# Kernel optimization log

Hardware: AMD Instinct MI355X
Metric: run time of the kernel (lower is better)

## Reference

```python
import jax, jax.numpy as jnp
import numpy as np
import math

N = 5000; K = 30; E = N * K
C_S, C_Z, C_A = 256, 128, 16
H, DH, P, L = 4, 64, 8, 4
NUM_AA = 21
NUM_RBF = 16; D_MIN, D_MAX = 2.0, 22.0
EPS = 1e-8

def _ln(x):
    mu = jnp.mean(x, -1, keepdims=True)
    var = jnp.mean((x - mu) ** 2, -1, keepdims=True)
    return (x - mu) * jax.lax.rsqrt(var + 1e-5)

def _inv_apply(rot, trans, x):
    # rigid invert_apply: R^T (x - t); rot [n,3,3], trans [n,3], x [n,p,3]
    return jnp.einsum('nji,npj->npi', rot, x - trans[:, None, :])

def _rbf(d):
    mu = jnp.linspace(D_MIN, D_MAX, NUM_RBF)
    sigma = (D_MAX - D_MIN) / NUM_RBF
    return jnp.exp(-(((d[..., None] - mu) / sigma) ** 2))

def _dihedral_feats(bb):
    X = bb.reshape(-1, 3)  # [3N,3] N,CA,C chain
    dX = X[1:] - X[:-1]
    U = dX / (jnp.linalg.norm(dX, axis=-1, keepdims=True) + EPS)
    u2, u1, u0 = U[:-2], U[1:-1], U[2:]
    n2 = jnp.cross(u2, u1); n2 = n2 / (jnp.linalg.norm(n2, axis=-1, keepdims=True) + EPS)
    n1 = jnp.cross(u1, u0); n1 = n1 / (jnp.linalg.norm(n1, axis=-1, keepdims=True) + EPS)
    cosD = jnp.clip(jnp.sum(n2 * n1, -1), -1 + 1e-7, 1 - 1e-7)
    D = jnp.sign(jnp.sum(u2 * n1, -1)) * jnp.arccos(cosD)
    D = jnp.pad(D, (1, 2)).reshape(-1, 3)  # [N,3]
    return jnp.concatenate([jnp.cos(D), jnp.sin(D)], -1)  # [N,6]

def _virtual_cb(n, ca, c):
    b = ca - n; cc = c - ca; a = jnp.cross(b, cc)
    return -0.58273431 * a + 0.56802827 * b - 0.54067466 * cc + ca

def _prep(seq, atom14, rot, trans, res_mask, mgm_mask, noising_mask, atom14_exists, edge_index, atom_tab):
    res_f = res_mask.astype(jnp.float32)
    mgm_f = mgm_mask.astype(jnp.float32)
    bb = atom14[:, :3]
    dih = _dihedral_feats(bb)
    seq_oh = jax.nn.one_hot(seq, NUM_AA)
    node_vec = _inv_apply(rot, trans, atom14[:, :4])  # [N,4,3]
    node_raw = jnp.concatenate([dih, mgm_f[:, None], seq_oh * mgm_f[:, None], node_vec.reshape(N, -1)], -1) * res_f[:, None]
    sc = jnp.where(jnp.arange(14) >= 4, mgm_f[:, None], 1.0)  # zero hidden side-chain atoms
    am_f = jnp.where(jnp.arange(14) >= 4, mgm_mask[:, None], atom14_exists).astype(jnp.float32)
    atom_raw = atom_tab[seq] * sc[..., None]  # [N,14,9]
    dsti, srci = edge_index[0], edge_index[1]
    nsrc = noising_mask[srci].astype(jnp.float32); ndst = noising_mask[dsti].astype(jnp.float32)
    cb = _virtual_cb(bb[:, 0], bb[:, 1], bb[:, 2])
    bb4 = jnp.concatenate([bb, cb[:, None]], 1)  # [N,4,3]
    dist = jnp.linalg.norm(bb4[srci][:, :, None] - bb4[dsti][:, None, :] + EPS, axis=-1)  # [E,4,4]
    rbf = _rbf(dist).reshape(E, -1)  # [E,256]
    dpos = (dsti - srci).astype(jnp.float32)
    freq = jnp.exp(jnp.arange(0, 16, 2, dtype=jnp.float32) * (-math.log(10000.0) / 16))
    ang = dpos[:, None] * freq
    pe = jnp.concatenate([jnp.cos(ang), jnp.sin(ang)], -1)  # [E,16]
    bb_local = _inv_apply(rot, trans, bb4)
    src_local = bb_local[srci].reshape(E, -1) * (1 - nsrc)[:, None]
    dst_in_src = jnp.einsum('eji,epj->epi', rot[srci], bb4[dsti] - trans[srci][:, None, :]).reshape(E, -1) * (1 - ndst)[:, None]
    edge_mask = res_mask[srci] & res_mask[dsti]
    edge_raw = jnp.concatenate([ndst[:, None], nsrc[:, None], seq_oh[srci] * (1 - nsrc)[:, None], seq_oh[dsti] * (1 - ndst)[:, None], rbf, pe, src_local, dst_in_src], -1) * edge_mask.astype(jnp.float32)[:, None]
    return node_raw, edge_raw, atom_raw, res_f, am_f, edge_mask

def _mlp3(x, W1, W2, W3):
    return _ln(jax.nn.relu(jax.nn.relu(x @ W1) @ W2) @ W3)

def _net(node_raw, edge_raw, atom_raw, res_f, am_f, edge_mask, rot, trans, edge_index, Wn1, Wn2, Wn3, Wez1, Wez2, Wez3, Wa1, Wa2, Wa3, Wq, Wk, Wv, Wqp, Wkp, Wb, gamma, Wo, Wau, Wt1, Wt2, Wne, We1, We2, Wp1, Wp2, Wmu, Wlv):
    s = _mlp3(node_raw, Wn1, Wn2, Wn3)    # [N,256]
    z = _mlp3(edge_raw, Wez1, Wez2, Wez3) # [E,128]
    af = _mlp3(atom_raw, Wa1, Wa2, Wa3)   # [N,14,16]
    dsti, srci = edge_index[0], edge_index[1]
    em_f = edge_mask.astype(jnp.float32)
    w_pt = math.sqrt(2.0 / (9 * P)); w_l = math.sqrt(1.0 / 3.0)
    for l in range(L):
        q = (s @ Wq[l]).reshape(N, H, DH); k = (s @ Wk[l]).reshape(N, H, DH); v = (s @ Wv[l]).reshape(N, H, DH)
        qp = (s @ Wqp[l]).reshape(N, H, P, 3); kp = (s @ Wkp[l]).reshape(N, H, P, 3)
        qg = jnp.einsum('nij,nhpj->nhpi', rot, qp) + trans[:, None, None, :]
        kg = jnp.einsum('nij,nhpj->nhpi', rot, kp) + trans[:, None, None, :]
        logits = (jnp.sum(q[dsti] * k[srci], -1) * (w_l / math.sqrt(DH))
                  + w_l * (z @ Wb[l])
                  - 0.5 * w_pt * jax.nn.softplus(gamma[l]) * jnp.sum((qg[dsti] - kg[srci]) ** 2, (-2, -1)))
        logits = jnp.where(edge_mask[:, None], logits, -1e9)
        m = jax.ops.segment_max(logits, dsti, num_segments=N)
        a = jnp.exp(logits - m[dsti]) * em_f[:, None]
        a = a / (jax.ops.segment_sum(a, dsti, num_segments=N) + 1e-9)[dsti]
        ov = jax.ops.segment_sum(a[..., None] * v[srci], dsti, num_segments=N).reshape(N, -1)
        og = jax.ops.segment_sum(a[..., None, None] * kg[srci], dsti, num_segments=N)
        ol = jnp.einsum('nji,nhpj->nhpi', rot, og - trans[:, None, None, :])
        on = jnp.sqrt(jnp.sum(ol ** 2, -1) + EPS)
        s = _ln(s + jnp.concatenate([ov, ol.reshape(N, -1), on.reshape(N, -1)], -1) @ Wo[l])
        af = _ln(af + jnp.concatenate([af, jnp.broadcast_to(s[:, None, :], (N, 14, C_S))], -1) @ Wau[l])
        s = _ln(s + jax.nn.relu(s @ Wt1[l]) @ Wt2[l]) * res_f[:, None]
        h = s @ Wne[l]
        z = _ln(jax.nn.relu(jnp.concatenate([z, h[dsti], h[srci]], -1) @ We1[l]) @ We2[l]) * em_f[:, None]
        af = _ln(af + jax.nn.relu(af @ Wp1[l]) @ Wp2[l]) * am_f[..., None]
    return jnp.concatenate([s @ Wmu, s @ Wlv], -1)  # [N,512] = [mu | logvar]

def setup_inputs():
    ks = jax.random.split(jax.random.key(0), 40)
    w = lambda i, shp: jax.random.normal(ks[i], shp, dtype=jnp.float32) * 0.02
    return {
        'seq': jax.random.randint(ks[0], (N,), 0, NUM_AA, dtype=jnp.int32),
        'atom14': jax.random.normal(ks[1], (N, 14, 3), dtype=jnp.float32) * 3.0,
        'rot': jax.random.normal(ks[2], (N, 3, 3), dtype=jnp.float32),
        'trans': jax.random.normal(ks[3], (N, 3), dtype=jnp.float32) * 3.0,
        'res_mask': jnp.ones((N,), dtype=bool),
        'mgm_mask': jax.random.bernoulli(ks[4], 0.5, (N,)),
        'noising_mask': jax.random.bernoulli(ks[5], 0.5, (N,)),
        'atom14_exists': jnp.ones((N, 14), dtype=bool),
        'edge_index': jax.random.randint(ks[6], (2, E), 0, N, dtype=jnp.int32),
        'atom_tab': jax.random.uniform(ks[7], (NUM_AA + 1, 14, 9), dtype=jnp.float32),
        'Wn1': w(8, (40, 512)), 'Wn2': w(9, (512, 512)), 'Wn3': w(10, (512, 256)),
        'Wez1': w(11, (340, 256)), 'Wez2': w(12, (256, 256)), 'Wez3': w(13, (256, 128)),
        'Wa1': w(14, (9, 32)), 'Wa2': w(15, (32, 32)), 'Wa3': w(16, (32, 16)),
        'Wq': w(17, (L, 256, 256)), 'Wk': w(18, (L, 256, 256)), 'Wv': w(19, (L, 256, 256)),
        'Wqp': w(20, (L, 256, H * P * 3)), 'Wkp': w(21, (L, 256, H * P * 3)),
        'Wb': w(22, (L, 128, H)), 'gamma': w(23, (L, H)),
        'Wo': w(24, (L, H * (DH + 4 * P), 256)), 'Wau': w(25, (L, C_A + C_S, C_A)),
        'Wt1': w(26, (L, 256, 256)), 'Wt2': w(27, (L, 256, 256)),
        'Wne': w(28, (L, 256, 128)), 'We1': w(29, (L, 384, 256)), 'We2': w(30, (L, 256, 128)),
        'Wp1': w(31, (L, 16, 16)), 'Wp2': w(32, (L, 16, 16)),
        'Wmu': w(33, (256, 256)), 'Wlv': w(34, (256, 256)),
    }

def reference(seq, atom14, rot, trans, res_mask, mgm_mask, noising_mask, atom14_exists, edge_index, atom_tab, Wn1, Wn2, Wn3, Wez1, Wez2, Wez3, Wa1, Wa2, Wa3, Wq, Wk, Wv, Wqp, Wkp, Wb, gamma, Wo, Wau, Wt1, Wt2, Wne, We1, We2, Wp1, Wp2, Wmu, Wlv):
    prep = _prep(seq, atom14, rot, trans, res_mask, mgm_mask, noising_mask, atom14_exists, edge_index, atom_tab)
    return _net(*prep, rot, trans, edge_index, Wn1, Wn2, Wn3, Wez1, Wez2, Wez3, Wa1, Wa2, Wa3, Wq, Wk, Wv, Wqp, Wkp, Wb, gamma, Wo, Wau, Wt1, Wt2, Wne, We1, We2, Wp1, Wp2, Wmu, Wlv)
```

## Files before the change

kernel.cpp:

```cpp
#include <hip/hip_runtime.h>
#include <hip/hip_bf16.h>

#define NR 5000
#define EE 150000
#define NA14 (NR*14)
#define EPSF 1e-8f

typedef unsigned short ushort;
typedef __attribute__((ext_vector_type(8))) short bf16x8;
typedef __attribute__((ext_vector_type(4))) float f32x4;

#define GLDS16(gp, lp) __builtin_amdgcn_global_load_lds( \
    (__attribute__((address_space(1))) void*)(gp), \
    (__attribute__((address_space(3))) void*)(lp), 16, 0, 0)

static __device__ __forceinline__ float wsum64(float v) {
#pragma unroll
  for (int o = 1; o < 64; o <<= 1) v += __shfl_xor(v, o, 64);
  return v;
}
static __device__ __forceinline__ ushort f2b(float f) {
  union { float f; unsigned u; } x; x.f = f;
  unsigned r = (x.u + 0x7FFF + ((x.u >> 16) & 1)) >> 16;
  return (ushort)r;
// ... 312 lines not shown
  const int ks0 = (sl - rl0 - (rl0 >> 2)) & 3;
  const int ks1 = (sl - rl1 - (rl1 >> 2)) & 3;
  int ar0 = bm + rl0; if (ar0 >= M) ar0 = M - 1;
  int ar1 = bm + rl1; if (ar1 >= M) ar1 = M - 1;
  const ushort* gA0 = A + (size_t)ar0 * lda + ks0 * 8;
  const ushort* gA1 = A + (size_t)ar1 * lda + ks1 * 8;
  const ushort* gB0 = BT + (size_t)(bn + rl0) * Kd + ks0 * 8;
  const ushort* gB1 = BT + (size_t)(bn + rl1) * Kd + ks1 * 8;

  auto stage = [&](int buf, int k0) {
    GLDS16(gA0 + k0, &As[buf][rl0][sl][0]);
    GLDS16(gB0 + k0, &Bs[buf][rl0][sl][0]);
    GLDS16(gA1 + k0, &As[buf][rl1][sl][0]);
    GLDS16(gB1 + k0, &Bs[buf][rl1][sl][0]);
  };

  f32x4 zero4 = {0.f, 0.f, 0.f, 0.f};
  f32x4 acc[4][4];
#pragma unroll
  for (int i = 0; i < 4; ++i)
#pragma unroll
    for (int j = 0; j < 4; ++j) acc[i][j] = zero4;

  stage(0, 0);
  asm volatile("s_waitcnt vmcnt(0)" ::: "memory");
  __builtin_amdgcn_s_barrier();

  const int nt = Kd >> 5;
  for (int t = 0; t < nt; ++t) {
    int cur = t & 1;
    if (t + 1 < nt) stage(cur ^ 1, (t + 1) << 5);
    {
      const int ksr = lane >> 4, lr = lane & 15;
      bf16x8 af[4], bf[4];
#pragma unroll
      for (int i = 0; i < 4; ++i) {
        int row = wm + i*16 + lr;
        int sa = (ksr + row + (row >> 2)) & 3;
        af[i] = *reinterpret_cast<const bf16x8*>(&As[cur][row][sa][0]);
      }
#pragma unroll
      for (int j = 0; j < 4; ++j) {
        int col = wn + j*16 + lr;
        int sb = (ksr + col + (col >> 2)) & 3;
        bf[j] = *reinterpret_cast<const bf16x8*>(&Bs[cur][col][sb][0]);
      }
#pragma unroll
      for (int i = 0; i < 4; ++i)
#pragma unroll
        for (int j = 0; j < 4; ++j)
          acc[i][j] = __builtin_amdgcn_mfma_f32_16x16x32_bf16(af[i], bf[j], acc[i][j], 0, 0, 0);
    }
    asm volatile("s_waitcnt vmcnt(0) lgkmcnt(0)" ::: "memory");
    __builtin_amdgcn_s_barrier();
  }

  int lr = lane & 15, lg = lane >> 4;
  if (LNZ) {
    float* stats = (float*)As;
#pragma unroll
    for (int i = 0; i < 4; ++i) {
#pragma unroll
      for (int rg = 0; rg < 4; ++rg) {
        float ps = 0.f, pq = 0.f;
#pragma unroll
        for (int j = 0; j < 4; ++j) {
          float v = b2f(f2b(acc[i][j][rg]));
          ps += v; pq += v * v;
        }
#pragma unroll
        for (int o = 1; o < 16; o <<= 1) {
          ps += __shfl_xor(ps, o, 64);
          pq += __shfl_xor(pq, o, 64);
        }
        if (lr == 0) {
          int row = wm + i*16 + lg*4 + rg;
          stats[(row * 2 + (wn >> 6)) * 2 + 0] = ps;
          stats[(row * 2 + (wn >> 6)) * 2 + 1] = pq;
        }
      }
    }
    __syncthreads();
#pragma unroll
    for (int i = 0; i < 4; ++i) {
#pragma unroll
      for (int rg = 0; rg < 4; ++rg) {
        int row = wm + i*16 + lg*4 + rg;
        int m = bm + row;
        float s0 = stats[(row*2 + 0)*2 + 0] + stats[(row*2 + 1)*2 + 0];
        float q0 = stats[(row*2 + 0)*2 + 1] + stats[(row*2 + 1)*2 + 1];
        float mu = s0 * (1.f / 128.f);
        float var = q0 * (1.f / 128.f) - mu * mu;
        float rs = rsqrtf(var + 1e-5f);
        if (m < M) {
          float sc = lnsc ? lnsc[m] : 1.f;
#pragma unroll
          for (int j = 0; j < 4; ++j) {
            int cc = wn + j*16 + lr;
            float v = b2f(f2b(acc[i][j][rg]));
            Cb[(size_t)m * 128 + cc] = f2b((v - mu) * rs * sc);
          }
        }
      }
    }
  } else if (PERMOUT) {
    const int pc = bn + wn + lr * 4;
#pragma unroll
    for (int i = 0; i < 4; ++i) {
#pragma unroll
      for (int rg = 0; rg < 4; ++rg) {
        int m = bm + wm + i*16 + lg*4 + rg;
        if (m >= M) continue;
        float v0 = acc[i][0][rg], v1 = acc[i][1][rg];
        float v2 = acc[i][2][rg], v3 = acc[i][3][rg];
        if (EPADD) {
          int de = dsti[m], se = srci[m];
          uint2 hd = *reinterpret_cast<const uint2*>(HD + (size_t)de * Ncols + pc);
          uint2 hs = *reinterpret_cast<const uint2*>(HS + (size_t)se * Ncols + pc);
          v0 += blo(hd.x) + blo(hs.x);
          v1 += bhi(hd.x) + bhi(hs.x);
          v2 += blo(hd.y) + blo(hs.y);
          v3 += bhi(hd.y) + bhi(hs.y);
        }
        if (RELU) {
          v0 = fmaxf(v0, 0.f); v1 = fmaxf(v1, 0.f);
          v2 = fmaxf(v2, 0.f); v3 = fmaxf(v3, 0.f);
        }
        uint2 p;
        p.x = (unsigned)f2b(v0) | ((unsigned)f2b(v1) << 16);
        p.y = (unsigned)f2b(v2) | ((unsigned)f2b(v3) << 16);
        *reinterpret_cast<uint2*>(Cb + (size_t)m * Ncols + pc) = p;
      }
    }
  } else {
#pragma unroll
    for (int i = 0; i < 4; ++i) {
#pragma unroll
      for (int rg = 0; rg < 4; ++rg) {
        int m = bm + wm + i*16 + lg*4 + rg;
        if (m >= M) continue;
#pragma unroll
        for (int j = 0; j < 4; ++j) {
          int cc = bn + wn + j*16 + lr;
          float v = acc[i][j][rg];
          if (RELU) v = fmaxf(v, 0.f);
          if (OUTBF) Cb[(size_t)m * Ncols + cc] = f2b(v);
          else       Cf[(size_t)m * Ncols + cc] = v;
        }
      }
    }
  }
}

__global__ void k_gemm(const float* __restrict__ A, const float* __restrict__ B,
                       float* __restrict__ C, int M, int Ncols, int Kd,
                       int ldc, int coff, int relu) {
  __shared__ float As[16][68];
  __shared__ float Bs[16][64];
  const int tid = threadIdx.x;
  const int bm = blockIdx.x * 64;
  const int bn = blockIdx.y * 64;
  const int tm = tid >> 4;
  const int tn = tid & 15;
  const int arow = tid >> 2;
  const int akq = (tid & 3) << 2;
  const int brow = tid >> 4;
  const int bcol = (tid & 15) << 2;
  float acc[4][4] = {{0.f}};
  const int am = bm + arow;
  for (int k0 = 0; k0 < Kd; k0 += 16) {
    float av[4];
#pragma unroll
    for (int j = 0; j < 4; ++j) {
      int k = k0 + akq + j;
      av[j] = (am < M && k < Kd) ? A[(size_t)am * Kd + k] : 0.f;
    }
#pragma unroll
    for (int j = 0; j < 4; ++j) As[akq + j][arow] = av[j];
    int kb = k0 + brow;
    float bv[4];
    if (kb < Kd) {
#pragma unroll
      for (int j = 0; j < 4; ++j) {
        int c = bn + bcol + j;
        bv[j] = (c < Ncols) ? B[(size_t)kb * Ncols + c] : 0.f;
      }
    } else { bv[0]=bv[1]=bv[2]=bv[3]=0.f; }
    *reinterpret_cast<float4*>(&Bs[brow][bcol]) = make_float4(bv[0],bv[1],bv[2],bv[3]);
    __syncthreads();
#pragma unroll
    for (int kk = 0; kk < 16; ++kk) {
      float4 a4 = *reinterpret_cast<const float4*>(&As[kk][tm << 2]);
      float4 b4 = *reinterpret_cast<const float4*>(&Bs[kk][tn << 2]);
      float aa[4] = {a4.x, a4.y, a4.z, a4.w};
      float bb[4] = {b4.x, b4.y, b4.z, b4.w};
#pragma unroll
      for (int i = 0; i < 4; ++i)
#pragma unroll
        for (int j = 0; j < 4; ++j)
          acc[i][j] = fmaf(aa[i], bb[j], acc[i][j]);
    }
    __syncthreads();
  }
#pragma unroll
  for (int i = 0; i < 4; ++i) {
    int m = bm + (tm << 2) + i;
    if (m >= M) continue;
#pragma unroll
    for (int j = 0; j < 4; ++j) {
      int c = bn + (tn << 2) + j;
      if (c >= Ncols) continue;
      float v = acc[i][j];
      if (relu) v = fmaxf(v, 0.f);
      C[(size_t)m * ldc + coff + c] = v;
    }
  }
}

__global__ void k_small_gemm(const float* __restrict__ A, const float* __restrict__ B,
                             float* __restrict__ C, int M, int Ncols, int Kd, int relu) {
  __shared__ float Ws[1024];
  int t = threadIdx.x;
  int nw = Kd * Ncols;
  for (int i = t; i < nw; i += 256) Ws[i] = B[i];
  __syncthreads();
  int rpb = 256 / Ncols;
  int r = blockIdx.x * rpb + t / Ncols;
  int c = t - (t / Ncols) * Ncols;
  if (r >= M || t >= rpb * Ncols) return;
  const float* a = A + (size_t)r * Kd;
  float s = 0.f;
  for (int k = 0; k < Kd; ++k) s = fmaf(a[k], Ws[k * Ncols + c], s);
  if (relu) s = fmaxf(s, 0.f);
  C[(size_t)r * Ncols + c] = s;
}

__global__ void k_ln(float* __restrict__ dst, ushort* __restrict__ dstb,
                     const float* __restrict__ res, const float* __restrict__ x,
                     const float* __restrict__ rowscale, int M) {
  int r = blockIdx.x * 4 + (threadIdx.x >> 6);
  if (r >= M) return;
  int l = threadIdx.x & 63;
  size_t base = (size_t)r * 256 + l * 4;
  float4 v = *reinterpret_cast<const float4*>(x + base);
  if (res) {
    float4 rv = *reinterpret_cast<const float4*>(res + base);
    v.x += rv.x; v.y += rv.y; v.z += rv.z; v.w += rv.w;
  }
  float s = wsum64(v.x + v.y + v.z + v.w);
  float mu = s * (1.f / 256.f);
  float d0 = v.x-mu, d1 = v.y-mu, d2 = v.z-mu, d3 = v.w-mu;
  float s2 = wsum64(d0*d0 + d1*d1 + d2*d2 + d3*d3);
  float rs = rsqrtf(s2 * (1.f / 256.f) + 1e-5f);
  float sc = rowscale ? rowscale[r] : 1.f;
  float o0 = d0*rs*sc, o1 = d1*rs*sc, o2 = d2*rs*sc, o3 = d3*rs*sc;
  *reinterpret_cast<float4*>(dst + base) = make_float4(o0, o1, o2, o3);
  if (dstb) {
    uint2 p;
    p.x = (unsigned)f2b(o0) | ((unsigned)f2b(o1) << 16);
    p.y = (unsigned)f2b(o2) | ((unsigned)f2b(o3) << 16);
    *reinterpret_cast<uint2*>(dstb + base) = p;
  }
}

__global__ void k_ln16(float* __restrict__ af, int M) {
  int r = blockIdx.x * 256 + threadIdx.x;
  if (r >= M) return;
  float x[16]; float s = 0.f;
#pragma unroll
  for (int j = 0; j < 16; ++j) { x[j] = af[(size_t)r*16 + j]; s += x[j]; }
  float mu = s * (1.f/16.f);
  float v = 0.f;
#pragma unroll
  for (int j = 0; j < 16; ++j) { float d = x[j]-mu; v += d*d; }
  float rs = rsqrtf(v * (1.f/16.f) + 1e-5f);
#pragma unroll
  for (int j = 0; j < 16; ++j) af[(size_t)r*16 + j] = (x[j]-mu)*rs;
}


__global__ void k_qg(const float* __restrict__ rot, const float* __restrict__ trans,
                     const float* __restrict__ pp,
                     float* __restrict__ qg, float* __restrict__ kg) {
  int idx = blockIdx.x * 256 + threadIdx.x;
  if (idx >= NR * 64) return;
  int n = idx >> 6; int w = (idx >> 5) & 1; int hp = idx & 31;
  const float* src = pp + (size_t)n*256 + (w ? 96 : 0) + hp*3;
  float* dstp = (w ? kg : qg) + (size_t)n*96 + hp*3;
  const float* R = rot + (size_t)n*9;
  const float* t = trans + (size_t)n*3;
  float s0 = src[0], s1 = src[1], s2 = src[2];
#pragma unroll
  for (int i = 0; i < 3; ++i)
    dstp[i] = R[i*3+0]*s0 + R[i*3+1]*s1 + R[i*3+2]*s2 + t[i];
}

__global__ __launch_bounds__(256) void k_attn2(
    const int* __restrict__ offs, const int* __restrict__ eord,
    const int* __restrict__ srci, const float* __restrict__ emf,
    const ushort* __restrict__ qkv, const ushort* __restrict__ z,
    const float* __restrict__ qg, const float* __restrict__ kg,
    const float* __restrict__ WbT, const float* __restrict__ coef,
    ushort* __restrict__ catb, float* __restrict__ og) {
  int n = blockIdx.x * 4 + (threadIdx.x >> 6);
  if (n >= NR) return;
  int l = threadIdx.x & 63;
  int hh = l >> 4, t = l & 15;
  int e0 = offs[n], e1 = offs[n+1];
  const float wl = 0.57735026918962576f;
  const float qk_scale = wl * 0.125f;
  uint2 qw = *reinterpret_cast<const uint2*>(qkv + (size_t)n*768 + hh*64 + t*4);
  float q0 = blo(qw.x), q1 = bhi(qw.x), q2 = blo(qw.y), q3 = bhi(qw.y);
  float qg1 = qg[(size_t)n*96 + hh*24 + t];
  float qg2 = (t < 8) ? qg[(size_t)n*96 + hh*24 + t + 16] : 0.f;
  float cf = coef[hh];
  int hg0 = l / 24;
  int hg1 = (64 + l) / 24;

  float m[4] = {-1e30f,-1e30f,-1e30f,-1e30f};
  float den[4] = {0.f,0.f,0.f,0.f};
  float accv[4] = {0.f,0.f,0.f,0.f};
  float acg0 = 0.f, acg1 = 0.f;

  int e = 0, s = 0;
  if (e0 < e1) { e = eord[e0]; s = srci[e]; }
  for (int i = e0; i < e1; ++i) {
    int e_nxt = 0, s_nxt = 0;
    if (i + 1 < e1) { e_nxt = eord[i + 1]; s_nxt = srci[e_nxt]; }
    float em = emf[e];
    uint2 kw = *reinterpret_cast<const uint2*>(qkv + (size_t)s*768 + 256 + hh*64 + t*4);
    float acc = qk_scale * (q0*blo(kw.x) + q1*bhi(kw.x) + q2*blo(kw.y) + q3*bhi(kw.y));
    {
      uint4 zw = *reinterpret_cast<const uint4*>(z + (size_t)e*128 + t*8);
      const float* wb = WbT + hh*128 + t*8;
      float4 w0 = *reinterpret_cast<const float4*>(wb);
      float4 w1 = *reinterpret_cast<const float4*>(wb + 4);
      acc += wl * (blo(zw.x)*w0.x + bhi(zw.x)*w0.y + blo(zw.y)*w0.z + bhi(zw.y)*w0.w
                 + blo(zw.z)*w1.x + bhi(zw.z)*w1.y + blo(zw.w)*w1.z + bhi(zw.w)*w1.w);
    }
    {
      float dq = qg1 - kg[(size_t)s*96 + hh*24 + t];
      acc -= cf * dq * dq;
      if (t < 8) {
        float dq2 = qg2 - kg[(size_t)s*96 + hh*24 + t + 16];
        acc -= cf * dq2 * dq2;
      }
    }
#pragma unroll
    for (int o = 1; o < 16; o <<= 1) acc += __shfl_xor(acc, o, 64);
    float a[4], r[4];
#pragma unroll
    for (int h = 0; h < 4; ++h) {
      float vh = __shfl(acc, h*16, 64);
      float lg = (em > 0.f) ? vh : -1e9f;
      float mn = m[h];
      r[h] = 1.f;
      if (lg > mn) { r[h] = expf(mn - lg); mn = lg; m[h] = mn; }
      a[h] = expf(lg - mn) * em;
      den[h] = den[h] * r[h] + a[h];
    }
#pragma unroll
    for (int j = 0; j < 4; ++j)
      accv[j] = accv[j] * r[j] + a[j] * b2f(qkv[(size_t)s*768 + 512 + j*64 + l]);
    acg0 = acg0 * r[hg0] + a[hg0] * kg[(size_t)s*96 + l];
    if (l < 32) acg1 = acg1 * r[hg1] + a[hg1] * kg[(size_t)s*96 + 64 + l];
    e = e_nxt; s = s_nxt;
  }
#pragma unroll
  for (int j = 0; j < 4; ++j)
    catb[(size_t)n*384 + j*64 + l] = f2b(accv[j] / (den[j] + 1e-9f));
  og[(size_t)n*96 + l] = acg0 / (den[hg0] + 1e-9f);
  if (l < 32) og[(size_t)n*96 + 64 + l] = acg1 / (den[hg1] + 1e-9f);
}

__global__ void k_olon(const float* __restrict__ rot, const float* __restrict__ trans,
                       const float* __restrict__ og, ushort* __restrict__ catb) {
  int idx = blockIdx.x * 256 + threadIdx.x;
  if (idx >= NR * 32) return;
  int n = idx >> 5, hp = idx & 31;
  const float* R = rot + (size_t)n*9;
  const float* t = trans + (size_t)n*3;
  const float* o = og + (size_t)n*96 + hp*3;
  float d0 = o[0]-t[0], d1 = o[1]-t[1], d2 = o[2]-t[2];
  float ol[3];
#pragma unroll
  for (int i = 0; i < 3; ++i)
    ol[i] = R[0*3+i]*d0 + R[1*3+i]*d1 + R[2*3+i]*d2;
  ushort* cp = catb + (size_t)n*384;
  cp[256 + hp*3 + 0] = f2b(ol[0]);
  cp[256 + hp*3 + 1] = f2b(ol[1]);
  cp[256 + hp*3 + 2] = f2b(ol[2]);
  cp[352 + hp] = f2b(sqrtf(ol[0]*ol[0] + ol[1]*ol[1] + ol[2]*ol[2] + EPSF));
}

__global__ void k_af_wau(float* __restrict__ af, const float* __restrict__ WauA,
                         const float* __restrict__ t1) {
  __shared__ float W[256];
  int t = threadIdx.x;
  W[t] = WauA[t];
  __syncthreads();
  int r = blockIdx.x * 256 + t;
  if (r >= NA14) return;
  int n = r / 14;
  float x[16], y[16];
#pragma unroll
  for (int j = 0; j < 16; ++j) x[j] = af[(size_t)r*16 + j];
#pragma unroll
  for (int j = 0; j < 16; ++j) y[j] = t1[(size_t)n*16 + j];
#pragma unroll
  for (int k = 0; k < 16; ++k) {
    float xv = x[k];
#pragma unroll
    for (int j = 0; j < 16; ++j) y[j] = fmaf(xv, W[k*16 + j], y[j]);
  }
  float v[16]; float s = 0.f;
#pragma unroll
  for (int j = 0; j < 16; ++j) { v[j] = x[j] + y[j]; s += v[j]; }
  float mu = s * (1.f/16.f);
  float var = 0.f;
#pragma unroll
  for (int j = 0; j < 16; ++j) { float d = v[j]-mu; var += d*d; }
  float rs = rsqrtf(var * (1.f/16.f) + 1e-5f);
#pragma unroll
  for (int j = 0; j < 16; ++j) af[(size_t)r*16 + j] = (v[j]-mu)*rs;
}

__global__ void k_af_p(float* __restrict__ af, const float* __restrict__ Wp1,
                       const float* __restrict__ Wp2, const float* __restrict__ amf) {
  __shared__ float W1[256], W2[256];
  int t = threadIdx.x;
  W1[t] = Wp1[t]; W2[t] = Wp2[t];
  __syncthreads();
  int r = blockIdx.x * 256 + t;
  if (r >= NA14) return;
  float x[16];
#pragma unroll
  for (int j = 0; j < 16; ++j) x[j] = af[(size_t)r*16 + j];
  float h1[16];
#pragma unroll
  for (int j = 0; j < 16; ++j) h1[j] = 0.f;
#pragma unroll
  for (int k = 0; k < 16; ++k) {
    float xv = x[k];
#pragma unroll
    for (int j = 0; j < 16; ++j) h1[j] = fmaf(xv, W1[k*16 + j], h1[j]);
  }
#pragma unroll
  for (int j = 0; j < 16; ++j) h1[j] = fmaxf(h1[j], 0.f);
  float h2[16];
#pragma unroll
  for (int j = 0; j < 16; ++j) h2[j] = 0.f;
#pragma unroll
  for (int k = 0; k < 16; ++k) {
    float xv = h1[k];
#pragma unroll
    for (int j = 0; j < 16; ++j) h2[j] = fmaf(xv, W2[k*16 + j], h2[j]);
  }
  float v[16]; float s = 0.f;
#pragma unroll
  for (int j = 0; j < 16; ++j) { v[j] = x[j] + h2[j]; s += v[j]; }
  float mu = s * (1.f/16.f);
  float var = 0.f;
#pragma unroll
  for (int j = 0; j < 16; ++j) { float d = v[j]-mu; var += d*d; }
  float rs = rsqrtf(var * (1.f/16.f) + 1e-5f);
  float am = amf[r];
#pragma unroll
  for (int j = 0; j < 16; ++j) af[(size_t)r*16 + j] = (v[j]-mu)*rs*am;
}

__global__ void k_sentinel(float* __restrict__ out, float val) {
  if (threadIdx.x == 0 && blockIdx.x == 0) out[0] = val;
}


extern "C" void kernel_launch(void* const* d_in, const int* in_sizes, int n_in,
                              void* d_out, int out_size, void* d_ws, size_t ws_size,
                              hipStream_t stream) {
  (void)in_sizes; (void)n_in; (void)out_size;
  const int*   seq    = (const int*)  d_in[0];
  const float* atom14 = (const float*)d_in[1];
  const float* rot    = (const float*)d_in[2];
  const float* trans  = (const float*)d_in[3];
  const int*   rmask  = (const int*)  d_in[4];
  const int*   mgm    = (const int*)  d_in[5];
  const int*   nmask  = (const int*)  d_in[6];
  const int*   a14ex  = (const int*)  d_in[7];
  const int*   eidx   = (const int*)  d_in[8];
  const int*   dsti   = eidx;
  const int*   srci   = eidx + EE;
  const float* atab   = (const float*)d_in[9];
  const float* Wn1 = (const float*)d_in[10];
  const float* Wn2 = (const float*)d_in[11];
  const float* Wn3 = (const float*)d_in[12];
  const float* Wez1 = (const float*)d_in[13];
  const float* Wez2 = (const float*)d_in[14];
  const float* Wez3 = (const float*)d_in[15];
  const float* Wa1 = (const float*)d_in[16];
  const float* Wa2 = (const float*)d_in[17];
  const float* Wa3 = (const float*)d_in[18];
  const float* Wq  = (const float*)d_in[19];
  const float* Wk  = (const float*)d_in[20];
  const float* Wv  = (const float*)d_in[21];
  const float* Wqp = (const float*)d_in[22];
  const float* Wkp = (const float*)d_in[23];
  const float* Wb  = (const float*)d_in[24];
  const float* gam = (const float*)d_in[25];
  const float* Wo  = (const float*)d_in[26];
  const float* Wau = (const float*)d_in[27];
  const float* Wt1 = (const float*)d_in[28];
  const float* Wt2 = (const float*)d_in[29];
  const float* Wne = (const float*)d_in[30];
  const float* We1 = (const float*)d_in[31];
  const float* We2 = (const float*)d_in[32];
  const float* Wp1 = (const float*)d_in[33];
  const float* Wp2 = (const float*)d_in[34];
  const float* Wmu = (const float*)d_in[35];
  const float* Wlv = (const float*)d_in[36];
  float* out = (float*)d_out;

  float* ws = (float*)d_ws;
  size_t WSF = ws_size / sizeof(float);
  size_t off = 0;
  auto alloc = [&](size_t n) { n = (n + 3) & ~(size_t)3; float* p = ws + off; off += n; return p; };

  ushort* Zb  = (ushort*)alloc((size_t)EE * 64);
  float* S    = alloc((size_t)NR * 256);
  ushort* SB  = (ushort*)alloc((size_t)NR * 128);
  float* AF   = alloc((size_t)NA14 * 16);
  float* AMF  = alloc(NA14);
  float* EMF  = alloc(EE);
  float* LOG  = alloc((size_t)EE * 4);
  float* RESF = alloc(NR);
  float* DP   = alloc(3 * NR);
  float* BB4  = alloc((size_t)NR * 12);
  float* BBL  = alloc((size_t)NR * 12);
  ushort* NRAWB = (ushort*)alloc((size_t)NR * 32);
  float* ARAW = alloc((size_t)NA14 * 9);
  ushort* WezT1 = (ushort*)alloc(45056);
  ushort* WezT2 = (ushort*)alloc(32768);
  ushort* WezT3 = (ushort*)alloc(16384);
  ushort* We1zT = (ushort*)alloc(65536);
  ushort* We1dT = (ushort*)alloc(65536);
  ushort* We1sT = (ushort*)alloc(65536);
  ushort* We2T  = (ushort*)alloc(65536);
  ushort* WqkvT = (ushort*)alloc(393216);
  ushort* WppT  = (ushort*)alloc(131072);
  ushort* WoT   = (ushort*)alloc(196608);
  ushort* Wt1T  = (ushort*)alloc(131072);
  ushort* Wt2T  = (ushort*)alloc(131072);
  ushort* WneT  = (ushort*)alloc(65536);
  ushort* WmuLvT= (ushort*)alloc(65536);
  ushort* Wn1T  = (ushort*)alloc(16384);
  ushort* Wn2T  = (ushort*)alloc(131072);
  ushort* Wn3T  = (ushort*)alloc(65536);
  float* WBT  = alloc(2048);
  float* COEF = alloc(16);
  ushort* QKVB= (ushort*)alloc((size_t)NR * 384);
  float* PP   = alloc((size_t)NR * 256);
  float* QG   = alloc((size_t)NR * 96);
  float* KG   = alloc((size_t)NR * 96);
  ushort* CATB= (ushort*)alloc((size_t)NR * 192);
  float* OGb  = alloc((size_t)NR * 96);
  float* NBUF = alloc((size_t)NR * 256);
  ushort* HbB = (ushort*)alloc((size_t)NR * 64);
  ushort* HDb = (ushort*)alloc((size_t)NR * 128);
  ushort* HSb = (ushort*)alloc((size_t)NR * 128);
  float* T1   = alloc((size_t)NR * 16);
  ushort* NB1b = (ushort*)alloc((size_t)NR * 256);
  ushort* NB2b = (ushort*)alloc((size_t)NR * 256);
  ushort* TRHb = (ushort*)alloc((size_t)NR * 128);
  float* AH1  = alloc((size_t)NA14 * 32);
  float* AH2  = alloc((size_t)NA14 * 32);
  int* CNT  = (int*)alloc(NR);
  int* OFFS = (int*)alloc(NR + 1);
  int* EORD = (int*)alloc(EE);
  size_t fixedF = off;

  if (fixedF + (size_t)432 * 1024 > WSF) {
    k_sentinel<<<1, 64, 0, stream>>>(out, 1.0e6f * (float)(ws_size >> 20));
    return;
  }
  float* EAR = ws + fixedF;
  size_t arenaF = WSF - fixedF;
  int CH_P = (int)((arenaF / 432 > (size_t)EE) ? (size_t)EE : arenaF / 432);
  int CH_L = (int)((arenaF / 128 > (size_t)EE) ? (size_t)EE : arenaF / 128);
  ushort* ERb = (ushort*)EAR;
  ushort* B1b = ERb + (size_t)CH_P * 352;
  ushort* B2b = B1b + (size_t)CH_P * 256;
  ushort* EARb = (ushort*)EAR;
  (void)LOG;

  auto wT = [&](const float* W, ushort* WTp, int K, int N, int Kpad,
                long ss, long ds, int L, int perm) {
    long tot = (long)N * Kpad * L;
    k_wT<<<(int)((tot + 255) / 256), 256, 0, stream>>>(W, WTp, K, N, Kpad, ss, ds, L, perm);
  };

  wT(Wez1, WezT1, 340, 256, 352, 0, 0, 1, 0);
  wT(Wez2, WezT2, 256, 256, 256, 0, 0, 1, 1);
  wT(Wez3, WezT3, 256, 128, 256, 0, 0, 1, 1);
  wT(Wn1, Wn1T, 40, 512, 64, 0, 0, 1, 0);
  wT(Wn2, Wn2T, 512, 512, 512, 0, 0, 1, 1);
  wT(Wn3, Wn3T, 512, 256, 512, 0, 0, 1, 1);
  wT(We1,         We1zT, 128, 256, 128, 98304, 32768, 4, 0);
  wT(We1 + 32768, We1dT, 128, 256, 128, 98304, 32768, 4, 0);
  wT(We1 + 65536, We1sT, 128, 256, 128, 98304, 32768, 4, 0);
  wT(We2, We2T, 256, 128, 256, 32768, 32768, 4, 1);
  wT(Wo,  WoT,  384, 256, 384, 98304, 98304, 4, 0);
  wT(Wt1, Wt1T, 256, 256, 256, 65536, 65536, 4, 0);
  wT(Wt2, Wt2T, 256, 256, 256, 65536, 65536, 4, 1);
  wT(Wne, WneT, 256, 128, 256, 32768, 32768, 4, 0);
  wT(Wmu, WmuLvT, 256, 256, 256, 0, 0, 1, 0);
  wT(Wlv, WmuLvT + 65536, 256, 256, 256, 0, 0, 1, 0);
  wT(Wq,  WqkvT + 0,       256, 256, 256, 65536, 196608, 4, 0);
  wT(Wk,  WqkvT + 65536,   256, 256, 256, 65536, 196608, 4, 0);
  wT(Wv,  WqkvT + 131072,  256, 256, 256, 65536, 196608, 4, 0);
  wT(Wqp, WppT + 0,        256,  96, 256, 24576, 65536, 4, 0);
  wT(Wkp, WppT + 24576,    256,  96, 256, 24576, 65536, 4, 0);
  k_zero_us<<<(64*256*4 + 255)/256, 256, 0, stream>>>(WppT + 49152, 64*256, 65536, 4);
  k_wbT<<<8, 256, 0, stream>>>(Wb, WBT);
  k_coef<<<1, 64, 0, stream>>>(gam, COEF);

  k_masks<<<(NR + 255) / 256, 256, 0, stream>>>(rmask, RESF);
  k_dihedral<<<(3 * NR + 255) / 256, 256, 0, stream>>>(atom14, DP);
  k_bb4<<<(NR + 255) / 256, 256, 0, stream>>>(atom14, rot, trans, BB4, BBL);
  k_noderaw<<<NR, 64, 0, stream>>>(seq, atom14, rot, trans, DP, rmask, mgm, NRAWB);
  k_atomraw<<<(NA14 + 255) / 256, 256, 0, stream>>>(seq, mgm, a14ex, atab, ARAW, AMF);

  {
    dim3 g1((NR + 127) / 128, 4), g2((NR + 127) / 128, 4), g3((NR + 127) / 128, 2);
    k_mgemm<1,1,0,1,0><<<g1, 256, 0, stream>>>(NRAWB, Wn1T, nullptr, NB1b, NR, 512, 64, 64,
                                               nullptr, nullptr, nullptr, nullptr, nullptr);
    k_mgemm<1,1,0,1,0><<<g2, 256, 0, stream>>>(NB1b, Wn2T, nullptr, NB2b, NR, 512, 512, 512,
                                               nullptr, nullptr, nullptr, nullptr, nullptr);
    k_mgemm<0,0,0,0,0><<<g3, 256, 0, stream>>>(NB2b, Wn3T, NBUF, nullptr, NR, 256, 512, 512,
                                               nullptr, nullptr, nullptr, nullptr, nullptr);
  }
  k_ln<<<(NR + 3) / 4, 256, 0, stream>>>(S, SB, nullptr, NBUF, nullptr, NR);

  k_small_gemm<<<(NA14 + 7) / 8, 256, 0, stream>>>(ARAW, Wa1, AH1, NA14, 32, 9, 1);
  k_small_gemm<<<(NA14 + 7) / 8, 256, 0, stream>>>(AH1, Wa2, AH2, NA14, 32, 32, 1);
  k_small_gemm<<<(NA14 + 15) / 16, 256, 0, stream>>>(AH2, Wa3, AF, NA14, 16, 32, 0);
  k_ln16<<<(NA14 + 255) / 256, 256, 0, stream>>>(AF, NA14);

  k_zero_int<<<(NR + 255) / 256, 256, 0, stream>>>(CNT, NR);
  k_count<<<(EE + 255) / 256, 256, 0, stream>>>(dsti, CNT);
  k_scan<<<1, 256, 0, stream>>>(CNT, OFFS);
  k_zero_int<<<(NR + 255) / 256, 256, 0, stream>>>(CNT, NR);
  k_place<<<(EE + 255) / 256, 256, 0, stream>>>(dsti, OFFS, CNT, EORD);
  k_sortwave<<<NR, 64, 0, stream>>>(OFFS, EORD);

  for (int e0 = 0; e0 < EE; e0 += CH_P) {
    int cnt = (EE - e0 < CH_P) ? (EE - e0) : CH_P;
    k_edgeraw<<<(cnt + 3) / 4, 256, 0, stream>>>(dsti, srci, seq, rmask, nmask,
                                                 BB4, BBL, rot, trans, ERb, EMF, e0, cnt);
    dim3 g1((cnt + 127) / 128, 2), g2((cnt + 127) / 128, 2), g3((cnt + 127) / 128, 1);
    k_mgemm<1,1,0,1,0><<<g1, 256, 0, stream>>>(ERb, WezT1, nullptr, B1b, cnt, 256, 352, 352,
                                               nullptr, nullptr, nullptr, nullptr, nullptr);
    k_mgemm<1,1,0,1,0><<<g2, 256, 0, stream>>>(B1b, WezT2, nullptr, B2b, cnt, 256, 256, 256,
                                               nullptr, nullptr, nullptr, nullptr, nullptr);
    k_mgemm<0,1,0,0,1><<<g3, 256, 0, stream>>>(B2b, WezT3, nullptr, Zb + (size_t)e0 * 128,
                                               cnt, 128, 256, 256,
                                               nullptr, nullptr, nullptr, nullptr, nullptr);
  }

  for (int l = 0; l < 4; ++l) {
    const ushort* WqkvT_l = WqkvT + (size_t)l * 196608;
    const ushort* WppT_l  = WppT  + (size_t)l * 65536;
    const ushort* WoT_l = WoT + (size_t)l * 98304;
    const float* Wau_l = Wau + (size_t)l * 4352;
    const ushort* Wt1T_l = Wt1T + (size_t)l * 65536;
    const ushort* Wt2T_l = Wt2T + (size_t)l * 65536;
    const ushort* WneT_l = WneT + (size_t)l * 32768;
    const ushort* We1zT_l = We1zT + (size_t)l * 32768;
    const ushort* We1dT_l = We1dT + (size_t)l * 32768;
    const ushort* We1sT_l = We1sT + (size_t)l * 32768;
    const ushort* We2T_l = We2T + (size_t)l * 32768;
    const float* Wp1_l = Wp1 + (size_t)l * 256;
    const float* Wp2_l = Wp2 + (size_t)l * 256;

    {
      dim3 gq((NR + 127) / 128, 6);
      k_mgemm<0,1,0,0,0><<<gq, 256, 0, stream>>>(SB, WqkvT_l, nullptr, QKVB, NR, 768, 256, 256,
                                                 nullptr, nullptr, nullptr, nullptr, nullptr);
      dim3 gp((NR + 127) / 128, 2);
      k_mgemm<0,0,0,0,0><<<gp, 256, 0, stream>>>(SB, WppT_l, PP, nullptr, NR, 256, 256, 256,
                                                 nullptr, nullptr, nullptr, nullptr, nullptr);
    }
    k_qg<<<(NR * 64 + 255) / 256, 256, 0, stream>>>(rot, trans, PP, QG, KG);
    k_attn2<<<(NR + 3) / 4, 256, 0, stream>>>(OFFS, EORD, srci, EMF, QKVB, Zb, QG, KG,
                                              WBT + (size_t)l * 512, COEF + (size_t)l * 4,
                                              CATB, OGb);
    k_olon<<<(NR * 32 + 255) / 256, 256, 0, stream>>>(rot, trans, OGb, CATB);
    {
      dim3 g((NR + 127) / 128, 2);
      k_mgemm<0,0,0,0,0><<<g, 256, 0, stream>>>(CATB, WoT_l, NBUF, nullptr, NR, 256, 384, 384,
                                                nullptr, nullptr, nullptr, nullptr, nullptr);
    }
    k_ln<<<(NR + 3) / 4, 256, 0, stream>>>(S, SB, S, NBUF, nullptr, NR);
    {
      dim3 g((NR + 63) / 64, 1);
      k_gemm<<<g, 256, 0, stream>>>(S, Wau_l + 256, T1, NR, 16, 256, 16, 0, 0);
    }
    k_af_wau<<<(NA14 + 255) / 256, 256, 0, stream>>>(AF, Wau_l, T1);
    {
      dim3 g((NR + 127) / 128, 2);
      k_mgemm<1,1,0,1,0><<<g, 256, 0, stream>>>(SB, Wt1T_l, nullptr, TRHb, NR, 256, 256, 256,
                                                nullptr, nullptr, nullptr, nullptr, nullptr);
      k_mgemm<0,0,0,0,0><<<g, 256, 0, stream>>>(TRHb, Wt2T_l, NBUF, nullptr, NR, 256, 256, 256,
                                                nullptr, nullptr, nullptr, nullptr, nullptr);
    }
    k_ln<<<(NR + 3) / 4, 256, 0, stream>>>(S, SB, S, NBUF, RESF, NR);
    {
      dim3 g((NR + 127) / 128, 1);
      k_mgemm<0,1,0,0,0><<<g, 256, 0, stream>>>(SB, WneT_l, nullptr, HbB, NR, 128, 256, 256,
                                                nullptr, nullptr, nullptr, nullptr, nullptr);
    }
    {
      dim3 g((NR + 127) / 128, 2);
      k_mgemm<0,1,0,1,0><<<g, 256, 0, stream>>>(HbB, We1dT_l, nullptr, HDb, NR, 256, 128, 128,
                                                nullptr, nullptr, nullptr, nullptr, nullptr);
      k_mgemm<0,1,0,1,0><<<g, 256, 0, stream>>>(HbB, We1sT_l, nullptr, HSb, NR, 256, 128, 128,
                                                nullptr, nullptr, nullptr, nullptr, nullptr);
    }
    for (int e0 = 0; e0 < EE; e0 += CH_L) {
      int cnt = (EE - e0 < CH_L) ? (EE - e0) : CH_L;
      dim3 g1((cnt + 127) / 128, 2), g2((cnt + 127) / 128, 1);
      k_mgemm<1,1,1,1,0><<<g1, 256, 0, stream>>>(Zb + (size_t)e0 * 128, We1zT_l, nullptr, EARb,
                                                 cnt, 256, 128, 128,
                                                 HDb, HSb, dsti + e0, srci + e0, nullptr);
      k_mgemm<0,1,0,0,1><<<g2, 256, 0, stream>>>(EARb, We2T_l, nullptr, Zb + (size_t)e0 * 128,
                                                 cnt, 128, 256, 256,
                                                 nullptr, nullptr, nullptr, nullptr, EMF + e0);
    }
    k_af_p<<<(NA14 + 255) / 256, 256, 0, stream>>>(AF, Wp1_l, Wp2_l, AMF);
  }

  {
    dim3 g((NR + 127) / 128, 4);
    k_mgemm<0,0,0,0,0><<<g, 256, 0, stream>>>(SB, WmuLvT, out, nullptr, NR, 512, 256, 256,
                                              nullptr, nullptr, nullptr, nullptr, nullptr);
  }
}
```

Baseline: 1.842 ms.

## Split attention edge loop across two waves per node with LDS softmax merge

```diff
diff --git a/kernel.cpp b/kernel.cpp
--- a/kernel.cpp
+++ b/kernel.cpp
@@ -638,17 +638,22 @@
     const float* __restrict__ qg, const float* __restrict__ kg,
     const float* __restrict__ WbT, const float* __restrict__ coef,
     ushort* __restrict__ catb, float* __restrict__ og) {
-  int n = blockIdx.x * 4 + (threadIdx.x >> 6);
-  if (n >= NR) return;
-  int l = threadIdx.x & 63;
-  int hh = l >> 4, t = l & 15;
-  int e0 = offs[n], e1 = offs[n+1];
+  __shared__ float MS[2][2][8];
+  __shared__ float AV[2][2][4][64];
+  __shared__ float AG0[2][2][64];
+  __shared__ float AG1[2][2][32];
+  const int w = threadIdx.x >> 6;
+  const int ns = w >> 1, half = w & 1;
+  const int n = blockIdx.x * 2 + ns;
+  const int l = threadIdx.x & 63;
+  const int hh = l >> 4, t = l & 15;
+  const int e0 = offs[n], e1 = offs[n+1];
   const float wl = 0.57735026918962576f;
   const float qk_scale = wl * 0.125f;
-  uint2 qw = *reinterpret_cast<const uint2*>(qkv + (size_t)n*768 + hh*64 + t*4);
+  uint2 qw = *reinterpret_cast<const uint2*>(qkv + n*768 + hh*64 + t*4);
   float q0 = blo(qw.x), q1 = bhi(qw.x), q2 = blo(qw.y), q3 = bhi(qw.y);
-  float qg1 = qg[(size_t)n*96 + hh*24 + t];
-  float qg2 = (t < 8) ? qg[(size_t)n*96 + hh*24 + t + 16] : 0.f;
+  float qg1 = qg[n*96 + hh*24 + t];
+  float qg2 = (t < 8) ? qg[n*96 + hh*24 + t + 16] : 0.f;
   float cf = coef[hh];
   int hg0 = l / 24;
   int hg1 = (64 + l) / 24;
@@ -658,13 +663,20 @@
   float accv[4] = {0.f,0.f,0.f,0.f};
   float acg0 = 0.f, acg1 = 0.f;
 
+  int i = e0 + half;
   int e = 0, s = 0;
-  if (e0 < e1) { e = eord[e0]; s = srci[e]; }
-  for (int i = e0; i < e1; ++i) {
+  if (i < e1) {
+    e = __builtin_amdgcn_readfirstlane(eord[i]);
+    s = __builtin_amdgcn_readfirstlane(srci[e]);
+  }
+  for (; i < e1; i += 2) {
     int e_nxt = 0, s_nxt = 0;
-    if (i + 1 < e1) { e_nxt = eord[i + 1]; s_nxt = srci[e_nxt]; }
+    if (i + 2 < e1) {
+      e_nxt = __builtin_amdgcn_readfirstlane(eord[i + 2]);
+      s_nxt = __builtin_amdgcn_readfirstlane(srci[e_nxt]);
+    }
     float em = emf[e];
-    uint2 kw = *reinterpret_cast<const uint2*>(qkv + (size_t)s*768 + 256 + hh*64 + t*4);
+    uint2 kw = *reinterpret_cast<const uint2*>(qkv + s*768 + 256 + hh*64 + t*4);
     float acc = qk_scale * (q0*blo(kw.x) + q1*bhi(kw.x) + q2*blo(kw.y) + q3*bhi(kw.y));
     {
       uint4 zw = *reinterpret_cast<const uint4*>(z + (size_t)e*128 + t*8);
@@ -675,10 +687,10 @@
                  + blo(zw.z)*w1.x + bhi(zw.z)*w1.y + blo(zw.w)*w1.z + bhi(zw.w)*w1.w);
     }
     {
-      float dq = qg1 - kg[(size_t)s*96 + hh*24 + t];
+      float dq = qg1 - kg[s*96 + hh*24 + t];
       acc -= cf * dq * dq;
       if (t < 8) {
-        float dq2 = qg2 - kg[(size_t)s*96 + hh*24 + t + 16];
+        float dq2 = qg2 - kg[s*96 + hh*24 + t + 16];
         acc -= cf * dq2 * dq2;
       }
     }
@@ -697,16 +709,40 @@
     }
 #pragma unroll
     for (int j = 0; j < 4; ++j)
-      accv[j] = accv[j] * r[j] + a[j] * b2f(qkv[(size_t)s*768 + 512 + j*64 + l]);
-    acg0 = acg0 * r[hg0] + a[hg0] * kg[(size_t)s*96 + l];
-    if (l < 32) acg1 = acg1 * r[hg1] + a[hg1] * kg[(size_t)s*96 + 64 + l];
+      accv[j] = accv[j] * r[j] + a[j] * b2f(qkv[s*768 + 512 + j*64 + l]);
+    acg0 = acg0 * r[hg0] + a[hg0] * kg[s*96 + l];
+    if (l < 32) acg1 = acg1 * r[hg1] + a[hg1] * kg[s*96 + 64 + l];
     e = e_nxt; s = s_nxt;
   }
-#pragma unroll
-  for (int j = 0; j < 4; ++j)
-    catb[(size_t)n*384 + j*64 + l] = f2b(accv[j] / (den[j] + 1e-9f));
-  og[(size_t)n*96 + l] = acg0 / (den[hg0] + 1e-9f);
-  if (l < 32) og[(size_t)n*96 + 64 + l] = acg1 / (den[hg1] + 1e-9f);
+  if (l == 0) {
+#pragma unroll
+    for (int h = 0; h < 4; ++h) { MS[ns][half][h] = m[h]; MS[ns][half][4+h] = den[h]; }
+  }
+#pragma unroll
+  for (int j = 0; j < 4; ++j) AV[ns][half][j][l] = accv[j];
+  AG0[ns][half][l] = acg0;
+  if (l < 32) AG1[ns][half][l] = acg1;
+  __syncthreads();
+  if (half) return;
+  float rA[4], rB[4], dC[4];
+#pragma unroll
+  for (int h = 0; h < 4; ++h) {
+    float mA = MS[ns][0][h], mB = MS[ns][1][h];
+    float mC = fmaxf(mA, mB);
+    rA[h] = expf(mA - mC); rB[h] = expf(mB - mC);
+    dC[h] = MS[ns][0][4+h]*rA[h] + MS[ns][1][4+h]*rB[h];
+  }
+#pragma unroll
+  for (int j = 0; j < 4; ++j) {
+    float v = AV[ns][0][j][l]*rA[j] + AV[ns][1][j][l]*rB[j];
+    catb[(size_t)n*384 + j*64 + l] = f2b(v / (dC[j] + 1e-9f));
+  }
+  float g0 = AG0[ns][0][l]*rA[hg0] + AG0[ns][1][l]*rB[hg0];
+  og[(size_t)n*96 + l] = g0 / (dC[hg0] + 1e-9f);
+  if (l < 32) {
+    float g1 = AG1[ns][0][l]*rA[hg1] + AG1[ns][1][l]*rB[hg1];
+    og[(size_t)n*96 + 64 + l] = g1 / (dC[hg1] + 1e-9f);
+  }
 }
 
 __global__ void k_olon(const float* __restrict__ rot, const float* __restrict__ trans,
@@ -866,7 +902,6 @@
   float* AF   = alloc((size_t)NA14 * 16);
   float* AMF  = alloc(NA14);
   float* EMF  = alloc(EE);
-  float* LOG  = alloc((size_t)EE * 4);
   float* RESF = alloc(NR);
   float* DP   = alloc(3 * NR);
   float* BB4  = alloc((size_t)NR * 12);
@@ -925,7 +960,6 @@
   ushort* B1b = ERb + (size_t)CH_P * 352;
   ushort* B2b = B1b + (size_t)CH_P * 256;
   ushort* EARb = (ushort*)EAR;
-  (void)LOG;
 
   auto wT = [&](const float* W, ushort* WTp, int K, int N, int Kpad,
                 long ss, long ds, int L, int perm) {
@@ -1025,9 +1059,9 @@
                                                  nullptr, nullptr, nullptr, nullptr, nullptr);
     }
     k_qg<<<(NR * 64 + 255) / 256, 256, 0, stream>>>(rot, trans, PP, QG, KG);
-    k_attn2<<<(NR + 3) / 4, 256, 0, stream>>>(OFFS, EORD, srci, EMF, QKVB, Zb, QG, KG,
-                                              WBT + (size_t)l * 512, COEF + (size_t)l * 4,
-                                              CATB, OGb);
+    k_attn2<<<NR / 2, 256, 0, stream>>>(OFFS, EORD, srci, EMF, QKVB, Zb, QG, KG,
+                                        WBT + (size_t)l * 512, COEF + (size_t)l * 4,
+                                        CATB, OGb);
     k_olon<<<(NR * 32 + 255) / 256, 256, 0, stream>>>(rot, trans, OGb, CATB);
     {
       dim3 g((NR + 127) / 128, 2);
```

New measurement: 1.820 ms. Within noise of the previous version (-1.2%).
